# Performance work log

Hardware: AMD Instinct MI355X
Metric: run time of the kernel (lower is better)

Reference implementation:

```python
import jax, jax.numpy as jnp
import numpy as np

B, T, N, K, IB, O = 128, 16, 65536, 8, 256, 10

def setup_inputs() -> dict:
    key = jax.random.key(0)
    ks = jax.random.split(key, 8)
    x = jax.random.randint(ks[0], (B, T, IB), 0, 2, dtype=jnp.int32)          # boolean input bits per timestep
    adj_list = jax.random.randint(ks[1], (N, K), 0, N, dtype=jnp.int32)       # incoming neighbors, homogenized
    adj_mask = jnp.ones((N, K), dtype=jnp.int32)                               # validity mask (all valid here)
    lut = jax.random.randint(ks[2], (N, 2 ** K), 0, 2, dtype=jnp.int32)        # boolean lookup table per node
    init_state = jax.random.randint(ks[3], (N,), 0, 2, dtype=jnp.int32)        # 'random' init strategy
    w_in = jnp.arange(IB, dtype=jnp.int32)                                     # input-bit -> node index map
    w_readout = jax.random.normal(ks[4], (O, N), dtype=jnp.float32) * 0.01
    b_readout = jax.random.normal(ks[5], (O,), dtype=jnp.float32)
    return dict(x=x, adj_list=adj_list, adj_mask=adj_mask, lut=lut,
                init_state=init_state, w_in=w_in,
                w_readout=w_readout, b_readout=b_readout)

def _run_reservoir(x, adj_list, adj_mask, lut, init_state, w_in):
    # x: [B,T,IB] bits; returns final boolean state [B,N] (int32)
    powers = (2 ** jnp.arange(K, dtype=jnp.int32))[::-1]   # matches powers_of_2 flip
    node_idx = jnp.arange(N, dtype=jnp.int32)
    state0 = jnp.broadcast_to(init_state[None, :], (B, N)).astype(jnp.int32)

    def step(state, xt):
        # perturb input nodes with this timestep's bits (xor perturbation)
        state = state.at[:, w_in].set(jnp.bitwise_xor(state[:, w_in], xt))
        # gather incoming-neighbor states, mask padded slots: [B,N,K]
        neigh = jnp.take(state, adj_list, axis=1) * adj_mask
        # pack K bits into LUT index, MSB-first: [B,N]
        idx = jnp.sum(neigh * powers, axis=-1)
        # per-node boolean update via LUT gather
        new_state = lut[node_idx[None, :], idx]
        return new_state, None

    xT = jnp.swapaxes(x, 0, 1)  # [T,B,IB]
    final, _ = jax.lax.scan(step, state0, xT)
    return final

def reference(x, adj_list, adj_mask, lut, init_state, w_in, w_readout, b_readout):
    final = _run_reservoir(x, adj_list, adj_mask, lut, init_state, w_in)
    logits = final.astype(jnp.float32) @ w_readout.T + b_readout  # [B,O]
    return jax.nn.sigmoid(logits)
```

## Files before the change

### kernel.cpp

```cpp
#include <hip/hip_runtime.h>
#include <stdint.h>

#define NN     65536
#define KK     8
#define BB     128
#define TT     16
#define IBITS  256
#define OO     10

#define ZIDX         (NN + IBITS)
#define SBUF_ENTRIES (NN + IBITS + 1)
#define RCHUNKS 512
#define RNODES  128

__device__ __forceinline__ uint32_t bmask(uint32_t w, int off) {
  return (uint32_t)__builtin_amdgcn_sbfe((int)w, off, 1);
}
__device__ __forceinline__ uint32_t mux(uint32_t s, uint32_t hi, uint32_t lo) {
  return ((hi ^ lo) & s) ^ lo;
}

template<int D, int BASE> struct Sh7 {
  static __device__ __forceinline__ uint32_t eval(const uint32_t (&L)[4],
                                                  const uint32_t (&xv)[7]) {
    uint32_t lo = Sh7<D - 1, BASE>::eval(L, xv);
    uint32_t hi = Sh7<D - 1, BASE + (1 << (D - 1))>::eval(L, xv);
    return mux(xv[D - 1], hi, lo);
  }
};
template<int BASE> struct Sh7<2, BASE> {
  static __device__ __forceinline__ uint32_t eval(const uint32_t (&L)[4],
                                                  const uint32_t (&xv)[7]) {
    const uint32_t lw = L[BASE >> 5];
    const uint32_t c0 = bmask(lw, (BASE & 31) + 0);
    const uint32_t c1 = bmask(lw, (BASE & 31) + 1);
    const uint32_t c2 = bmask(lw, (BASE & 31) + 2);
    const uint32_t c3 = bmask(lw, (BASE & 31) + 3);
    const uint32_t t0 = mux(xv[0], c1, c0);
    const uint32_t t1 = mux(xv[0], c3, c2);
    return mux(xv[1], t1, t0);
  }
};

#define PB_LUT   2048
#define PB_MADJ  2048
#define PB_X     64
#define PB_STATE 256
#define PREP_BLOCKS (PB_LUT + PB_MADJ + PB_X + PB_STATE)

__global__ __launch_bounds__(256) void prep_kernel(
    const int* __restrict__ lut, const int* __restrict__ adj,
    const int* __restrict__ adjm, const int* __restrict__ x,
    const int* __restrict__ init,
    uint32_t* __restrict__ luttt, int* __restrict__ madj,
    uint32_t* __restrict__ xvecw, uint4* __restrict__ sA, uint4* __restrict__ sB) {
  const int b = blockIdx.x, t = threadIdx.x;
  if (b < PB_LUT) {
    const int g = b * 256 + t;
    const int n = g >> 3, w = g & 7;
    const int4* lut4 = (const int4*)lut;
    uint32_t val = 0;
#pragma unroll
    for (int q = 0; q < 8; ++q) {
      int4 v = lut4[n * 64 + w * 8 + q];
      val |= (uint32_t)(v.x & 1) << (4 * q + 0);
      val |= (uint32_t)(v.y & 1) << (4 * q + 1);
      val |= (uint32_t)(v.z & 1) << (4 * q + 2);
      val |= (uint32_t)(v.w & 1) << (4 * q + 3);
    }
    luttt[g] = val;
  } else if (b < PB_LUT + PB_MADJ) {
    const int g = (b - PB_LUT) * 256 + t;
    int a = adj[g];
    int m = adjm[g] & 1;
    madj[g] = m ? ((a < IBITS) ? a + NN : a) : ZIDX;
  } else if (b < PB_LUT + PB_MADJ + PB_X) {
    const int g = (b - PB_LUT - PB_MADJ) * 256 + t;
    const int tt = g >> 10, rest = g & 1023, i = rest >> 2, bq = rest & 3;
    uint32_t wv = 0;
#pragma unroll
    for (int bl = 0; bl < 32; ++bl) {
      int bb = bq * 32 + bl;
      wv |= (uint32_t)(x[(bb * TT + tt) * IBITS + i] & 1) << bl;
    }
    xvecw[(tt * IBITS + i) * 4 + bq] = wv;
  } else {
    const int n = (b - PB_LUT - PB_MADJ - PB_X) * 256 + t;
    uint32_t m = 0u - (uint32_t)(init[n] & 1);
    uint4 s = make_uint4(m, m, m, m);
    sA[n] = s;
    if (n < IBITS) {
      uint32_t wv[4] = {0, 0, 0, 0};
#pragma unroll
      for (int bb = 0; bb < BB; ++bb) {
        uint32_t bit = (uint32_t)(x[(bb * TT + 0) * IBITS + n] & 1);
        wv[bb >> 5] |= bit << (bb & 31);
      }
      sA[NN + n] = make_uint4(s.x ^ wv[0], s.y ^ wv[1], s.z ^ wv[2], s.w ^ wv[3]);
    }
    if (n == 0) {
      uint4 z = make_uint4(0, 0, 0, 0);
      sA[ZIDX] = z;
      sB[ZIDX] = z;
    }
  }
}

__global__ __launch_bounds__(256, 8) void step_kernel(const uint32_t* __restrict__ sinw,
                                                      uint32_t* __restrict__ soutw,
                                                      const uint4* __restrict__ luttt,
                                                      const int* __restrict__ madj,
                                                      const uint32_t* __restrict__ xnextw) {
  const int g = blockIdx.x * 256 + threadIdx.x;
  const int n = g >> 3;
  const int w = (g >> 1) & 3;
  const int h = g & 1;
  const int4* madj4 = (const int4*)madj;
  int4 a0 = madj4[n * 2 + 0], a1 = madj4[n * 2 + 1];
  uint4 lh = luttt[n * 2 + h];
  const uint32_t L[4] = {lh.x, lh.y, lh.z, lh.w};
  const int ia[8] = {a0.x, a0.y, a0.z, a0.w, a1.x, a1.y, a1.z, a1.w};
  uint32_t xv[7];
#pragma unroll
  for (int j = 0; j < 7; ++j)
    xv[j] = sinw[(ia[7 - j] << 2) + w];
  const uint32_t x7 = sinw[(ia[0] << 2) + w];
  const uint32_t rsub = Sh7<7, 0>::eval(L, xv);
  const uint32_t rpart = __shfl_xor(rsub, 1, 64);
  const uint32_t lo = h ? rpart : rsub;
  const uint32_t hi = h ? rsub : rpart;
  const uint32_t r = mux(x7, hi, lo);
  if (h == 0) {
    soutw[(n << 2) + w] = r;
  } else if (xnextw != nullptr && n < IBITS) {
    soutw[((NN + n) << 2) + w] = r ^ xnextw[(n << 2) + w];
  }
}

__global__ __launch_bounds__(256) void readout_kernel(const uint32_t* __restrict__ statew,
                                                      const float* __restrict__ w,
                                                      float* __restrict__ part) {
  __shared__ uint32_t sw[64 * 4];
  __shared__ float wsm[OO * 64];
  const int c = blockIdx.x;
  const int t = threadIdx.x;
  const int b = t & 127, oh = t >> 7;
  const int word = b >> 5, sh = b & 31;
  float acc[5] = {0.f, 0.f, 0.f, 0.f, 0.f};
  for (int s = 0; s < 2; ++s) {
    const int base = c * RNODES + s * 64;
    __syncthreads();
    sw[t] = statew[base * 4 + t];
#pragma unroll
    for (int r = 0; r < 3; ++r) {
      int idx = r * 256 + t;
      if (idx < OO * 64) wsm[idx] = w[(idx >> 6) * NN + base + (idx & 63)];
    }
    __syncthreads();
#pragma unroll 8
    for (int j = 0; j < 64; ++j) {
      uint32_t m = 0u - ((sw[j * 4 + word] >> sh) & 1u);
#pragma unroll
      for (int q = 0; q < 5; ++q) {
        uint32_t wv = __float_as_uint(wsm[(oh * 5 + q) * 64 + j]) & m;
        acc[q] += __uint_as_float(wv);
      }
    }
  }
#pragma unroll
  for (int q = 0; q < 5; ++q)
    part[(c * BB + b) * OO + oh * 5 + q] = acc[q];
}

__global__ __launch_bounds__(256) void finalize_kernel(const float* __restrict__ part,
                                                       const float* __restrict__ bias,
                                                       float* __restrict__ out) {
  __shared__ float red[256];
  const int i = blockIdx.x;
  const int b = i / OO, o = i % OO;
  const int t = threadIdx.x;
  float s = part[(t * BB + b) * OO + o] + part[((t + 256) * BB + b) * OO + o];
  red[t] = s;
  __syncthreads();
  for (int h = 128; h > 0; h >>= 1) {
    if (t < h) red[t] += red[t + h];
    __syncthreads();
  }
  if (t == 0) out[b * OO + o] = 1.f / (1.f + __expf(-(red[0] + bias[o])));
}

extern "C" void kernel_launch(void* const* d_in, const int* in_sizes, int n_in,
                              void* d_out, int out_size, void* d_ws, size_t ws_size,
                              hipStream_t stream) {
  const int* x    = (const int*)d_in[0];
  const int* adj  = (const int*)d_in[1];
  const int* adjm = (const int*)d_in[2];
  const int* lut  = (const int*)d_in[3];
  const int* init = (const int*)d_in[4];
  const float* wro = (const float*)d_in[6];
  const float* bro = (const float*)d_in[7];
  float* out = (float*)d_out;

  char* ws = (char*)d_ws;
  const size_t SBUF = (size_t)SBUF_ENTRIES * 16;
  uint4* sA        = (uint4*)(ws);
  uint4* sB        = (uint4*)(ws + SBUF);
  uint32_t* xvecw  = (uint32_t*)(ws + 2 * SBUF);
  uint32_t* luttt  = (uint32_t*)(ws + 2 * SBUF + (size_t)TT * IBITS * 16);
  int* madj        = (int*)(ws + 2 * SBUF + (size_t)TT * IBITS * 16 + (size_t)NN * 32);
  float* part      = (float*)(ws + 2 * SBUF + (size_t)TT * IBITS * 16 + (size_t)NN * 64);

  hipLaunchKernelGGL(prep_kernel, dim3(PREP_BLOCKS), dim3(256), 0, stream,
                     lut, adj, adjm, x, init, luttt, madj, xvecw, sA, sB);

  for (int t = 0; t < TT; ++t) {
    const uint32_t* sin = (const uint32_t*)((t & 1) ? sB : sA);
    uint32_t* sout      = (uint32_t*)((t & 1) ? sA : sB);
    const uint32_t* xn  = (t + 1 < TT) ? (xvecw + (size_t)(t + 1) * IBITS * 4) : nullptr;
    hipLaunchKernelGGL(step_kernel, dim3((NN * 8) / 256), dim3(256), 0, stream,
                       sin, sout, (const uint4*)luttt, madj, xn);
  }
  hipLaunchKernelGGL(readout_kernel, dim3(RCHUNKS), dim3(256), 0, stream,
                     (const uint32_t*)sA, wro, part);
  hipLaunchKernelGGL(finalize_kernel, dim3(BB * OO), dim3(256), 0, stream, part, bro, out);
}
```

Before: 288.4 us.

## Fuse all timesteps into one persistent kernel with a hierarchical grid barrier

Replaces the sixteen per-timestep step_kernel launches with one kernel of 2048 blocks that loops over timesteps. Blocks synchronise through a two-level atomic counter barrier (64 leaf counters feeding one root), and neighbour indices and LUT words stay in registers across steps. This removes per-launch overhead and repeated loads of the adjacency and LUT data. In exchange it relies on all 2048 blocks being co-resident (256 threads, 8 blocks per CU) and adds atomic-load and barrier latency to every step.

```diff
diff --git a/kernel.cpp b/kernel.cpp
--- a/kernel.cpp
+++ b/kernel.cpp
@@ -13,11 +13,21 @@
 #define RCHUNKS 512
 #define RNODES  128
 
+#define SP_BLOCKS 2048
+#define LEAVES    64
+#define BPL       (SP_BLOCKS / LEAVES)
+
 __device__ __forceinline__ uint32_t bmask(uint32_t w, int off) {
   return (uint32_t)__builtin_amdgcn_sbfe((int)w, off, 1);
 }
 __device__ __forceinline__ uint32_t mux(uint32_t s, uint32_t hi, uint32_t lo) {
   return ((hi ^ lo) & s) ^ lo;
+}
+__device__ __forceinline__ uint32_t aload(const uint32_t* p) {
+  return __hip_atomic_load(p, __ATOMIC_RELAXED, __HIP_MEMORY_SCOPE_AGENT);
+}
+__device__ __forceinline__ void astore(uint32_t* p, uint32_t v) {
+  __hip_atomic_store(p, v, __ATOMIC_RELAXED, __HIP_MEMORY_SCOPE_AGENT);
 }
 
 template<int D, int BASE> struct Sh7 {
@@ -53,7 +63,8 @@
     const int* __restrict__ adjm, const int* __restrict__ x,
     const int* __restrict__ init,
     uint32_t* __restrict__ luttt, int* __restrict__ madj,
-    uint32_t* __restrict__ xvecw, uint4* __restrict__ sA, uint4* __restrict__ sB) {
+    uint32_t* __restrict__ xvecw, uint4* __restrict__ sA, uint4* __restrict__ sB,
+    uint32_t* __restrict__ ctrs) {
   const int b = blockIdx.x, t = threadIdx.x;
   if (b < PB_LUT) {
     const int g = b * 256 + t;
@@ -98,6 +109,7 @@
       }
       sA[NN + n] = make_uint4(s.x ^ wv[0], s.y ^ wv[1], s.z ^ wv[2], s.w ^ wv[3]);
     }
+    if (n < 4096) ctrs[n] = 0;
     if (n == 0) {
       uint4 z = make_uint4(0, 0, 0, 0);
       sA[ZIDX] = z;
@@ -106,11 +118,29 @@
   }
 }
 
-__global__ __launch_bounds__(256, 8) void step_kernel(const uint32_t* __restrict__ sinw,
-                                                      uint32_t* __restrict__ soutw,
-                                                      const uint4* __restrict__ luttt,
-                                                      const int* __restrict__ madj,
-                                                      const uint32_t* __restrict__ xnextw) {
+__device__ __forceinline__ void grid_barrier2(uint32_t* ctrs, uint32_t phase) {
+  __syncthreads();
+  if (threadIdx.x == 0) {
+    asm volatile("s_waitcnt vmcnt(0)" ::: "memory");
+    uint32_t* leaf = &ctrs[(blockIdx.x & (LEAVES - 1)) * 32];
+    uint32_t old = __hip_atomic_fetch_add(leaf, 1u, __ATOMIC_RELAXED,
+                                          __HIP_MEMORY_SCOPE_AGENT);
+    if (old == phase * BPL - 1) {
+      __hip_atomic_fetch_add(&ctrs[LEAVES * 32], 1u, __ATOMIC_RELAXED,
+                             __HIP_MEMORY_SCOPE_AGENT);
+    }
+    while (__hip_atomic_load(&ctrs[LEAVES * 32], __ATOMIC_RELAXED,
+                             __HIP_MEMORY_SCOPE_AGENT) < phase * LEAVES) {
+      __builtin_amdgcn_s_sleep(2);
+    }
+  }
+  __syncthreads();
+}
+
+__global__ __launch_bounds__(256, 8) void steps_fused(
+    uint32_t* __restrict__ sA, uint32_t* __restrict__ sB,
+    const uint4* __restrict__ luttt, const int* __restrict__ madj,
+    const uint32_t* __restrict__ xvecw, uint32_t* __restrict__ ctrs) {
   const int g = blockIdx.x * 256 + threadIdx.x;
   const int n = g >> 3;
   const int w = (g >> 1) & 3;
@@ -118,22 +148,35 @@
   const int4* madj4 = (const int4*)madj;
   int4 a0 = madj4[n * 2 + 0], a1 = madj4[n * 2 + 1];
   uint4 lh = luttt[n * 2 + h];
-  const uint32_t L[4] = {lh.x, lh.y, lh.z, lh.w};
+  uint32_t L[4] = {lh.x, lh.y, lh.z, lh.w};
   const int ia[8] = {a0.x, a0.y, a0.z, a0.w, a1.x, a1.y, a1.z, a1.w};
-  uint32_t xv[7];
-#pragma unroll
-  for (int j = 0; j < 7; ++j)
-    xv[j] = sinw[(ia[7 - j] << 2) + w];
-  const uint32_t x7 = sinw[(ia[0] << 2) + w];
-  const uint32_t rsub = Sh7<7, 0>::eval(L, xv);
-  const uint32_t rpart = __shfl_xor(rsub, 1, 64);
-  const uint32_t lo = h ? rpart : rsub;
-  const uint32_t hi = h ? rsub : rpart;
-  const uint32_t r = mux(x7, hi, lo);
-  if (h == 0) {
-    soutw[(n << 2) + w] = r;
-  } else if (xnextw != nullptr && n < IBITS) {
-    soutw[((NN + n) << 2) + w] = r ^ xnextw[(n << 2) + w];
+  uint32_t off[7];
+#pragma unroll
+  for (int j = 0; j < 7; ++j) off[j] = ((uint32_t)ia[7 - j] << 4) + ((uint32_t)w << 2);
+  const uint32_t off7 = ((uint32_t)ia[0] << 4) + ((uint32_t)w << 2);
+
+  uint32_t* cur = sA;
+  uint32_t* nxt = sB;
+#pragma unroll 1
+  for (int t = 0; t < TT; ++t) {
+#pragma unroll
+    for (int i = 0; i < 4; ++i) asm volatile("" : "+v"(L[i]));
+    const char* base = (const char*)cur;
+    uint32_t xv[7];
+#pragma unroll
+    for (int j = 0; j < 7; ++j)
+      xv[j] = aload((const uint32_t*)(base + off[j]));
+    const uint32_t x7 = aload((const uint32_t*)(base + off7));
+    const uint32_t rsub = Sh7<7, 0>::eval(L, xv);
+    const uint32_t rpart = __shfl_xor(rsub, 1, 64);
+    const uint32_t r = mux(x7, h ? rsub : rpart, h ? rpart : rsub);
+    if (h == 0) {
+      astore(&nxt[(n << 2) + w], r);
+    } else if (n < IBITS && t + 1 < TT) {
+      astore(&nxt[((NN + n) << 2) + w], r ^ xvecw[((t + 1) * IBITS + n) * 4 + w]);
+    }
+    uint32_t* tmp = cur; cur = nxt; nxt = tmp;
+    if (t + 1 < TT) grid_barrier2(ctrs, (uint32_t)(t + 1));
   }
 }
 
@@ -209,17 +252,15 @@
   uint32_t* luttt  = (uint32_t*)(ws + 2 * SBUF + (size_t)TT * IBITS * 16);
   int* madj        = (int*)(ws + 2 * SBUF + (size_t)TT * IBITS * 16 + (size_t)NN * 32);
   float* part      = (float*)(ws + 2 * SBUF + (size_t)TT * IBITS * 16 + (size_t)NN * 64);
+  uint32_t* ctrs   = (uint32_t*)(ws + 2 * SBUF + (size_t)TT * IBITS * 16 + (size_t)NN * 64
+                                 + (size_t)RCHUNKS * BB * OO * 4);
 
   hipLaunchKernelGGL(prep_kernel, dim3(PREP_BLOCKS), dim3(256), 0, stream,
-                     lut, adj, adjm, x, init, luttt, madj, xvecw, sA, sB);
-
-  for (int t = 0; t < TT; ++t) {
-    const uint32_t* sin = (const uint32_t*)((t & 1) ? sB : sA);
-    uint32_t* sout      = (uint32_t*)((t & 1) ? sA : sB);
-    const uint32_t* xn  = (t + 1 < TT) ? (xvecw + (size_t)(t + 1) * IBITS * 4) : nullptr;
-    hipLaunchKernelGGL(step_kernel, dim3((NN * 8) / 256), dim3(256), 0, stream,
-                       sin, sout, (const uint4*)luttt, madj, xn);
-  }
+                     lut, adj, adjm, x, init, luttt, madj, xvecw, sA, sB, ctrs);
+
+  hipLaunchKernelGGL(steps_fused, dim3(SP_BLOCKS), dim3(256), 0, stream,
+                     (uint32_t*)sA, (uint32_t*)sB, (const uint4*)luttt, madj, xvecw, ctrs);
+
   hipLaunchKernelGGL(readout_kernel, dim3(RCHUNKS), dim3(256), 0, stream,
                      (const uint32_t*)sA, wro, part);
   hipLaunchKernelGGL(finalize_kernel, dim3(BB * OO), dim3(256), 0, stream, part, bro, out);
```

New measurement: 374.3 us. 1.3x slower.
